# Performance work log

Hardware: AMD Instinct MI355X
Metric: run time of the kernel (lower is better)

## Reference

```python
import jax, jax.numpy as jnp
import numpy as np

B, N, C_IN, C_OUT = 32, 4096, 16, 64
EMB, LINK, WIN = 16, 3, 12


def setup_inputs() -> dict:
    key = jax.random.key(0)
    ks = jax.random.split(key, 7)
    s = lambda k, shape, sc=1.0: jax.random.normal(k, shape, dtype=jnp.float32) * sc
    return {
        "x": s(ks[0], (B, N, C_IN)),
        "x_window": s(ks[1], (B, WIN, N, C_IN)),
        "node_embeddings": s(ks[2], (N, EMB)),
        "weights_pool": s(ks[3], (EMB, LINK, C_IN, C_OUT), 0.1),
        "weights_window": s(ks[4], (EMB, C_IN, C_OUT), 0.1),
        "bias_pool": s(ks[5], (EMB, C_OUT), 0.1),
        "T": s(ks[6], (WIN,), 0.1),
    }


def reference(x, x_window, node_embeddings, weights_pool, weights_window, bias_pool, T):
    # Adaptive adjacency: softmax over rows of relu(E E^T)   [N, N]
    n = node_embeddings.shape[0]
    supports = jax.nn.softmax(
        jax.nn.relu(node_embeddings @ node_embeddings.T), axis=1)
    # Chebyshev polynomial hops: T0=I, T1=A, Tk = 2*A*T(k-1) - T(k-2)
    support_set = [jnp.eye(n, dtype=supports.dtype), supports]
    for _ in range(2, weights_pool.shape[1]):
        support_set.append(2.0 * (supports @ support_set[-1]) - support_set[-2])
    supports_k = jnp.stack(support_set, axis=0)  # [K, N, N]

    # Per-node weight generation from node embeddings
    weights = jnp.einsum('nd,dkio->nkio', node_embeddings, weights_pool)  # [N,K,Cin,Cout]
    bias = node_embeddings @ bias_pool  # [N, Cout]

    # Multi-hop spatial graph convolution
    x_g = jnp.einsum('knm,bmc->bnkc', supports_k, x)  # [B, N, K, Cin]
    x_gconv = jnp.einsum('bnki,nkio->bno', x_g, weights) + bias  # [B, N, Cout]

    # Temporal window transformation: time-mix with T, per-node weights
    x_w = jnp.einsum('btni,t->bni', x_window, T)  # [B, N, Cin]
    w_win = jnp.einsum('nd,dio->nio', node_embeddings, weights_window)  # [N,Cin,Cout]
    x_wconv = jnp.einsum('bni,nio->bno', x_w, w_win)  # [B, N, Cout]

    return x_gconv + x_wconv
```

## Files before the change

### kernel.cpp

```cpp
#include <hip/hip_runtime.h>
#include <hip/hip_bf16.h>

#define NN 4096
#define BB 32
#define CIN 16
#define COUT 64
#define EMB 16
#define KLINK 3
#define WWIN 12
#define BCIN (BB * CIN)
#define KSPLIT 4
#define KCHUNK (NN / KSPLIT)
#define NT (KCHUNK / 32)

typedef unsigned short ushort_t;
typedef __attribute__((ext_vector_type(8))) short bf16x8;
typedef __attribute__((ext_vector_type(4))) float f32x4;
typedef __attribute__((ext_vector_type(4))) unsigned short us4;
typedef __attribute__((ext_vector_type(8))) unsigned short us8;

static __device__ __forceinline__ ushort_t f2bf(float f) {
  union { float f; unsigned u; } v; v.f = f;
  const unsigned r = v.u + 0x7fffu + ((v.u >> 16) & 1u);
  return (ushort_t)(r >> 16);
}

__device__ __forceinline__ void gload16(const void* g, void* l) {
  __builtin_amdgcn_global_load_lds(
      (const __attribute__((address_space(1))) void*)g,
      (__attribute__((address_space(3))) void*)l, 16, 0, 0);
}

__global__ __launch_bounds__(256) void prep_kernel(
    const float* __restrict__ E, const float* __restrict__ Wp,
    const float* __restrict__ Wwp, const float* __restrict__ biasp,
    ushort_t* __restrict__ Ebf, ushort_t* __restrict__ Wpct,
    float* __restrict__ biasn, float* __restrict__ r) {
  const int gid = blockIdx.x * 256 + threadIdx.x;
  if (gid < NN) {
    r[gid] = 0.0f;
    const float* e = E + (size_t)gid * EMB;
    ushort_t* o = Ebf + (size_t)gid * 32;
    #pragma unroll
    for (int d = 0; d < 16; ++d) o[d] = f2bf(e[d]);
    #pragma unroll
    for (int d = 16; d < 32; ++d) o[d] = 0;
  } else if (gid < 2 * NN) {
    const int j = gid - NN;
    const int oo = j >> 6;
    const int i = j & 63;
    const int q = i >> 4;
    const int ii = i & 15;
    ushort_t* w = Wpct + (size_t)j * 32;
    #pragma unroll
    for (int d = 0; d < 16; ++d) {
      float v;
      if (q == 0)
        v = Wp[((size_t)(d * 3 + 0) * 16 + ii) * 64 + oo] -
            Wp[((size_t)(d * 3 + 2) * 16 + ii) * 64 + oo];
      else if (q == 1)
        v = Wp[((size_t)(d * 3 + 1) * 16 + ii) * 64 + oo];
      else if (q == 2)
        v = 2.0f * Wp[((size_t)(d * 3 + 2) * 16 + ii) * 64 + oo];
      else
        v = Wwp[((size_t)d * 16 + ii) * 64 + oo];
      w[d] = f2bf(v);
    }
    #pragma unroll
    for (int d = 16; d < 32; ++d) w[d] = 0;
  } else {
    const int t = gid - 2 * NN;
    if (t < NN * 16) {
      const int n = t >> 4;
      const int o4 = t & 15;
      const float4* bp4 = reinterpret_cast<const float4*>(biasp);
      float4 acc = make_float4(0.f, 0.f, 0.f, 0.f);
      #pragma unroll
      for (int d = 0; d < 16; ++d) {
        const float e = E[(size_t)n * EMB + d];
        const float4 b = bp4[d * 16 + o4];
        acc.x += e * b.x; acc.y += e * b.y; acc.z += e * b.z; acc.w += e * b.w;
      }
      *reinterpret_cast<float4*>(biasn + (size_t)n * 64 + o4 * 4) = acc;
    }
  }
}

__global__ __launch_bounds__(256) void uber_kernel(
    const ushort_t* __restrict__ Ebf, const ushort_t* __restrict__ Wpct,
    ushort_t* __restrict__ Wall, ushort_t* __restrict__ Pb,
    float* __restrict__ r,
    const float* __restrict__ x, const float* __restrict__ xw,
    const float* __restrict__ Tv,
    ushort_t* __restrict__ XtT, float* __restrict__ XW) {
  __shared__ ushort_t smem[6144];
  const int bid = blockIdx.x;
  const int tid = threadIdx.x;
  const int g = bid / 14;
  const int rm = bid - g * 14;

  if (rm < 4) {
    const int pidx = g * 4 + rm;
    const int row0 = (pidx >> 6) * 128;
    const int col0 = (pidx & 63) * 64;
    ushort_t* As = smem;
    ushort_t* Bs = smem + 4096;
    const int lane = tid & 63;
    const int wid = tid >> 6;
    const int wr = wid >> 1;
    const int wc = wid & 1;
    const int sr = tid >> 2;
    const int scs = (((tid & 3) ^ (sr & 3)) * 8);
    gload16(Ebf + (size_t)(row0 + sr) * 32 + scs, &As[tid * 8]);
    gload16(Ebf + (size_t)(row0 + 64 + sr) * 32 + scs, &As[2048 + tid * 8]);
    gload16(Ebf + (size_t)(col0 + sr) * 32 + scs, &Bs[tid * 8]);
    __syncthreads();

    const int kq = (lane >> 4) * 8;
    const int fr = lane & 15;
    bf16x8 af[4], bfr[2];
    #pragma unroll
    for (int i = 0; i < 4; ++i) {
      const int rr = wr * 64 + i * 16 + fr;
      af[i] = *reinterpret_cast<const bf16x8*>(&As[rr * 32 + (kq ^ ((rr & 3) * 8))]);
    }
    #pragma unroll
    for (int j = 0; j < 2; ++j) {
      const int rr = wc * 32 + j * 16 + fr;
      bfr[j] = *reinterpret_cast<const bf16x8*>(&Bs[rr * 32 + (kq ^ ((rr & 3) * 8))]);
    }
    f32x4 acc[4][2];
    #pragma unroll
    for (int i = 0; i < 4; ++i)
      #pragma unroll
      for (int j = 0; j < 2; ++j) acc[i][j] = (f32x4){0.f, 0.f, 0.f, 0.f};
    #pragma unroll
    for (int i = 0; i < 4; ++i)
      #pragma unroll
      for (int j = 0; j < 2; ++j)
        acc[i][j] = __builtin_amdgcn_mfma_f32_16x16x32_bf16(af[i], bfr[j],
                                                            acc[i][j], 0, 0, 0);
    float pv[4][2][4];
    #pragma unroll
    for (int i = 0; i < 4; ++i) {
      const int rg = row0 + wr * 64 + i * 16 + ((lane >> 4) << 2);
      #pragma unroll
      for (int j = 0; j < 2; ++j) {
        const int cg = col0 + wc * 32 + j * 16 + (lane & 15);
        us4 o;
        #pragma unroll
        for (int q = 0; q < 4; ++q) {
          const float p = __expf(fmaxf(acc[i][j][q], 0.0f) - 16.0f);
          pv[i][j][q] = p;
          o[q] = f2bf(p);
        }
        *reinterpret_cast<us4*>(&Pb[(size_t)cg * NN + rg]) = o;
      }
    }
    #pragma unroll
    for (int i = 0; i < 4; ++i) {
      const int rg = row0 + wr * 64 + i * 16 + ((lane >> 4) << 2);
      #pragma unroll
      for (int q = 0; q < 4; ++q) {
        float s = pv[i][0][q] + pv[i][1][q];
        s += __shfl_xor(s, 1, 64);
        s += __shfl_xor(s, 2, 64);
        s += __shfl_xor(s, 4, 64);
        s += __shfl_xor(s, 8, 64);
        if ((lane & 15) == 0) atomicAdd(&r[rg + q], s);
      }
    }
  } else if (rm < 8) {
    const int widx = g * 4 + (rm - 4);
    const int row0 = (widx >> 6) * 128;
    const int col0 = (widx & 63) * 64;
    ushort_t* As = smem;
    ushort_t* Bs = smem + 4096;
    const int lane = tid & 63;
    const int wid = tid >> 6;
    const int wr = wid >> 1;
    const int wc = wid & 1;
    const int sr = tid >> 2;
    const int scs = (((tid & 3) ^ (sr & 3)) * 8);
    gload16(Wpct + (size_t)(row0 + sr) * 32 + scs, &As[tid * 8]);
    gload16(Wpct + (size_t)(row0 + 64 + sr) * 32 + scs, &As[2048 + tid * 8]);
    gload16(Ebf + (size_t)(col0 + sr) * 32 + scs, &Bs[tid * 8]);
    __syncthreads();

    const int kq = (lane >> 4) * 8;
    const int fr = lane & 15;
    bf16x8 af[4], bfr[2];
    #pragma unroll
    for (int i = 0; i < 4; ++i) {
      const int rr = wr * 64 + i * 16 + fr;
      af[i] = *reinterpret_cast<const bf16x8*>(&As[rr * 32 + (kq ^ ((rr & 3) * 8))]);
    }
    #pragma unroll
    for (int j = 0; j < 2; ++j) {
      const int rr = wc * 32 + j * 16 + fr;
      bfr[j] = *reinterpret_cast<const bf16x8*>(&Bs[rr * 32 + (kq ^ ((rr & 3) * 8))]);
    }
    f32x4 acc[4][2];
    #pragma unroll
    for (int i = 0; i < 4; ++i)
      #pragma unroll
      for (int j = 0; j < 2; ++j) acc[i][j] = (f32x4){0.f, 0.f, 0.f, 0.f};
    #pragma unroll
    for (int i = 0; i < 4; ++i)
      #pragma unroll
      for (int j = 0; j < 2; ++j)
        acc[i][j] = __builtin_amdgcn_mfma_f32_16x16x32_bf16(af[i], bfr[j],
                                                            acc[i][j], 0, 0, 0);
    #pragma unroll
    for (int i = 0; i < 4; ++i) {
      const int rg = row0 + wr * 64 + i * 16 + ((lane >> 4) << 2);
      #pragma unroll
      for (int j = 0; j < 2; ++j) {
        const int cg = col0 + wc * 32 + j * 16 + (lane & 15);
        us4 o;
        o.x = f2bf(acc[i][j][0]);
        o.y = f2bf(acc[i][j][1]);
        o.z = f2bf(acc[i][j][2]);
        o.w = f2bf(acc[i][j][3]);
        *reinterpret_cast<us4*>(&Wall[(size_t)cg * NN + rg]) = o;
      }
    }
  } else if (rm < 10) {
    const int tidx = g * 2 + (rm - 8);
    const int lin = tidx * 256 + tid;
    const int c4 = (lin & 3) << 2;
    const int nn0 = ((lin >> 6) & 127) * 32 + ((lin >> 2) & 15);
    const int b = lin >> 13;
    float tv[WWIN];
    #pragma unroll
    for (int t = 0; t < WWIN; ++t) tv[t] = Tv[t];
    float4 a0 = make_float4(0.f, 0.f, 0.f, 0.f);
    float4 a1 = make_float4(0.f, 0.f, 0.f, 0.f);
    #pragma unroll 3
    for (int t = 0; t < WWIN; ++t) {
      const float4 v0 = *reinterpret_cast<const float4*>(
          xw + (((size_t)b * WWIN + t) * NN + nn0) * CIN + c4);
      const float4 v1 = *reinterpret_cast<const float4*>(
          xw + (((size_t)b * WWIN + t) * NN + nn0 + 16) * CIN + c4);
      a0.x += v0.x * tv[t]; a0.y += v0.y * tv[t];
      a0.z += v0.z * tv[t]; a0.w += v0.w * tv[t];
      a1.x += v1.x * tv[t]; a1.y += v1.y * tv[t];
      a1.z += v1.z * tv[t]; a1.w += v1.w * tv[t];
    }
    *reinterpret_cast<float4*>(XW + ((size_t)b * NN + nn0) * CIN + c4) = a0;
    *reinterpret_cast<float4*>(XW + ((size_t)b * NN + nn0 + 16) * CIN + c4) = a1;
  } else {
    const int txidx = g * 4 + (rm - 10);
    const int b = txidx >> 6;
    const int m0 = (txidx & 63) * 64;
    ushort_t (*T)[72] = reinterpret_cast<ushort_t(*)[72]>(smem);
    const int i = tid & 15;
    const int ml = tid >> 4;
    #pragma unroll
    for (int it = 0; it < 4; ++it) {
      const int m = m0 + ml + it * 16;
      T[i][ml + it * 16] = f2bf(x[((size_t)b * NN + m) * CIN + i]);
    }
    __syncthreads();
    if (tid < 128) {
      const int rr = tid >> 3;
      const int c8 = (tid & 7) * 8;
      const us8 v = *reinterpret_cast<const us8*>(&T[rr][c8]);
      *reinterpret_cast<us8*>(&XtT[(size_t)(b * CIN + rr) * NN + m0 + c8]) = v;
    }
  }
}

template <int CUR>
__device__ __forceinline__ void compute_tile(
    const ushort_t (&As)[3][128 * 32], const ushort_t (&Bs)[3][64 * 32],
    f32x4 (&acc)[4][2], int wr, int wc, int kq, int fr) {
  bf16x8 af[4], bfr[2];
  #pragma unroll
  for (int i = 0; i < 4; ++i) {
    const int rr = wr * 64 + i * 16 + fr;
    af[i] = *reinterpret_cast<const bf16x8*>(
        &As[CUR][rr * 32 + (kq ^ ((rr & 3) * 8))]);
  }
  #pragma unroll
  for (int j = 0; j < 2; ++j) {
    const int rr = wc * 32 + j * 16 + fr;
    bfr[j] = *reinterpret_cast<const bf16x8*>(
        &Bs[CUR][rr * 32 + (kq ^ ((rr & 3) * 8))]);
  }
  #pragma unroll
  for (int i = 0; i < 4; ++i)
    #pragma unroll
    for (int j = 0; j < 2; ++j)
      acc[i][j] = __builtin_amdgcn_mfma_f32_16x16x32_bf16(af[i], bfr[j],
                                                          acc[i][j], 0, 0, 0);
}

__global__ __launch_bounds__(256) void gemm_splitk_kernel(
    const ushort_t* __restrict__ Ag, const ushort_t* __restrict__ Bt,
    float* __restrict__ Cp, int lda, int ldb, int ldc) {
  __shared__ ushort_t As[3][128 * 32];
  __shared__ ushort_t Bs[3][64 * 32];
  const int tid = threadIdx.x;
  const int lane = tid & 63;
  const int wid = tid >> 6;
  const int wr = wid >> 1;
  const int wc = wid & 1;

  const int gx = gridDim.x, gy = gridDim.y;
  const int nwg = gx * gy * gridDim.z;
  int L = blockIdx.x + gx * (blockIdx.y + gy * blockIdx.z);
  L = (L & 7) * (nwg >> 3) + (L >> 3);
  const int bx = L % gx;
  const int by = (L / gx) % gy;
  const int bz = L / (gx * gy);

  const int row0 = by * 128;
  const int col0 = bx * 64;
  const int kbase = bz * KCHUNK;

  f32x4 acc[4][2];
  #pragma unroll
  for (int i = 0; i < 4; ++i)
    #pragma unroll
    for (int j = 0; j < 2; ++j) acc[i][j] = (f32x4){0.f, 0.f, 0.f, 0.f};

  const int sr = tid >> 2;
  const int scs = (((tid & 3) ^ (sr & 3)) * 8);
  const ushort_t* agp0 = Ag + (size_t)(row0 + sr) * lda + scs;
  const ushort_t* agp1 = Ag + (size_t)(row0 + 64 + sr) * lda + scs;
  const ushort_t* bgp  = Bt + (size_t)(col0 + sr) * ldb + scs;

  const int kq = (lane >> 4) * 8;
  const int fr = lane & 15;

#define STAGE(BUF, KB)                              \
  gload16(agp0 + (KB), &As[BUF][tid * 8]);          \
  gload16(agp1 + (KB), &As[BUF][2048 + tid * 8]);   \
  gload16(bgp + (KB), &Bs[BUF][tid * 8]);

#define PIPE_STEP(CUR, NB, TT)                                  \
  STAGE(NB, kbase + ((TT) + 2) * 32);                           \
  asm volatile("s_waitcnt vmcnt(6)" ::: "memory");              \
  __builtin_amdgcn_s_barrier();                                 \
  __builtin_amdgcn_sched_barrier(0);                            \
  compute_tile<CUR>(As, Bs, acc, wr, wc, kq, fr);               \
  __builtin_amdgcn_sched_barrier(0);                            \
  __builtin_amdgcn_s_barrier();

  STAGE(0, kbase);
  STAGE(1, kbase + 32);

  for (int tt = 0; tt < (NT - 2) / 3; ++tt) {
    const int t3 = tt * 3;
    PIPE_STEP(0, 2, t3 + 0);
    PIPE_STEP(1, 0, t3 + 1);
    PIPE_STEP(2, 1, t3 + 2);
  }
  asm volatile("s_waitcnt vmcnt(3)" ::: "memory");
  __builtin_amdgcn_s_barrier();
  __builtin_amdgcn_sched_barrier(0);
  compute_tile<0>(As, Bs, acc, wr, wc, kq, fr);
  __builtin_amdgcn_sched_barrier(0);
  __builtin_amdgcn_s_barrier();
  asm volatile("s_waitcnt vmcnt(0)" ::: "memory");
  __builtin_amdgcn_s_barrier();
  __builtin_amdgcn_sched_barrier(0);
  compute_tile<1>(As, Bs, acc, wr, wc, kq, fr);

#undef PIPE_STEP
#undef STAGE

  float* cpz = Cp + (size_t)bz * ((size_t)BCIN * NN);
  #pragma unroll
  for (int i = 0; i < 4; ++i) {
    const int rg = row0 + wr * 64 + i * 16 + ((lane >> 4) << 2);
    #pragma unroll
    for (int j = 0; j < 2; ++j) {
      const int cg = col0 + wc * 32 + j * 16 + (lane & 15);
      *reinterpret_cast<f32x4*>(&cpz[(size_t)cg * ldc + rg]) = acc[i][j];
    }
  }
}

__global__ __launch_bounds__(256) void reduce_y1_kernel(
    const float* __restrict__ Cp, const float* __restrict__ R,
    ushort_t* __restrict__ Y1T, ushort_t* __restrict__ Y1n) {
  __shared__ ushort_t T[64][72];
  const int n0 = blockIdx.x * 64;
  const int bc0 = blockIdx.y * 64;
  const int tid = threadIdx.x;
  const size_t SS = (size_t)BCIN * NN;
  #pragma unroll
  for (int q = 0; q < 4; ++q) {
    const int lin = tid + q * 256;
    const int bc = lin >> 4;
    const int nc = (lin & 15) * 4;
    const size_t base = (size_t)(bc0 + bc) * NN + n0 + nc;
    float4 s = *reinterpret_cast<const float4*>(Cp + base);
    #pragma unroll
    for (int z = 1; z < KSPLIT; ++z) {
      const float4 v = *reinterpret_cast<const float4*>(Cp + (size_t)z * SS + base);
      s.x += v.x; s.y += v.y; s.z += v.z; s.w += v.w;
    }
    const float4 rv = *reinterpret_cast<const float4*>(R + n0 + nc);
    us4 o;
    o.x = f2bf(s.x / rv.x); o.y = f2bf(s.y / rv.y);
    o.z = f2bf(s.z / rv.z); o.w = f2bf(s.w / rv.w);
    *reinterpret_cast<us4*>(&Y1T[base]) = o;
    *reinterpret_cast<us4*>(&T[bc][nc]) = o;
  }
  __syncthreads();
  #pragma unroll
  for (int t = 0; t < 2; ++t) {
    const int lin = tid + t * 256;
    const int nr = lin >> 3;
    const int ch = lin & 7;
    us8 v;
    #pragma unroll
    for (int e = 0; e < 8; ++e) v[e] = T[ch * 8 + e][nr];
    *reinterpret_cast<us8*>(&Y1n[(size_t)(n0 + nr) * BCIN + bc0 + ch * 8]) = v;
  }
}

__global__ __launch_bounds__(256) void reduce_y2_kernel(
    const float* __restrict__ Cp, ushort_t* __restrict__ Ct,
    const float* __restrict__ R) {
  const size_t e = ((size_t)blockIdx.x * 256 + threadIdx.x) << 2;
  const size_t SS = (size_t)BCIN * NN;
  float4 s = *reinterpret_cast<const float4*>(Cp + e);
  #pragma unroll
  for (int z = 1; z < KSPLIT; ++z) {
    const float4 v = *reinterpret_cast<const float4*>(Cp + (size_t)z * SS + e);
    s.x += v.x; s.y += v.y; s.z += v.z; s.w += v.w;
  }
  const float ri = 1.0f / R[e >> 9];
  s.x *= ri; s.y *= ri; s.z *= ri; s.w *= ri;
  us4 o;
  o.x = f2bf(s.x); o.y = f2bf(s.y); o.z = f2bf(s.z); o.w = f2bf(s.w);
  *reinterpret_cast<us4*>(Ct + e) = o;
}

__global__ __launch_bounds__(256) void combine_kernel(
    const float* __restrict__ x, const ushort_t* __restrict__ Y1n,
    const ushort_t* __restrict__ Y2n, const float* __restrict__ XW,
    const ushort_t* __restrict__ Wall, const float* __restrict__ biasn,
    float* __restrict__ out) {
  __shared__ ushort_t lds[4 * 6144];
  const int tid = threadIdx.x;
  const int lane = tid & 63;
  const int w = tid >> 6;
  ushort_t* Wl = lds + w * 6144;
  ushort_t* Vl = Wl + 4096;

  const int perm = ((lane >> 3) << 3) | ((lane & 7) ^ (lane >> 3));
  const int vb = lane >> 1;
  const int i0 = (lane & 1) * 8;

  for (int it = 0; it < 2; ++it) {
    const int n = blockIdx.x * 8 + w * 2 + it;
    asm volatile("s_waitcnt lgkmcnt(0)" ::: "memory");

    const ushort_t* wrow = Wall + (size_t)n * 4096;
    #pragma unroll
    for (int q = 0; q < 8; ++q)
      gload16(wrow + q * 512 + perm * 8, Wl + q * 512);

    const float4* xp = reinterpret_cast<const float4*>(
        x + ((size_t)vb * NN + n) * CIN + i0);
    const float4 xa = xp[0], xb = xp[1];
    const us8 y1 = *reinterpret_cast<const us8*>(Y1n + (size_t)n * BCIN + lane * 8);
    const us8 y2 = *reinterpret_cast<const us8*>(Y2n + (size_t)n * BCIN + lane * 8);
    const float4* xwp = reinterpret_cast<const float4*>(
        XW + ((size_t)vb * NN + n) * CIN + i0);
    const float4 wa = xwp[0], wb = xwp[1];
    us8 xv, wv;
    xv[0] = f2bf(xa.x); xv[1] = f2bf(xa.y); xv[2] = f2bf(xa.z); xv[3] = f2bf(xa.w);
    xv[4] = f2bf(xb.x); xv[5] = f2bf(xb.y); xv[6] = f2bf(xb.z); xv[7] = f2bf(xb.w);
    wv[0] = f2bf(wa.x); wv[1] = f2bf(wa.y); wv[2] = f2bf(wa.z); wv[3] = f2bf(wa.w);
    wv[4] = f2bf(wb.x); wv[5] = f2bf(wb.y); wv[6] = f2bf(wb.z); wv[7] = f2bf(wb.w);
    const int c0 = (lane & 1);
    const int vswz = vb & 7;
    *reinterpret_cast<us8*>(Vl + vb * 64 + (((c0 + 0) ^ vswz) << 3)) = xv;
    *reinterpret_cast<us8*>(Vl + vb * 64 + (((c0 + 2) ^ vswz) << 3)) = y1;
    *reinterpret_cast<us8*>(Vl + vb * 64 + (((c0 + 4) ^ vswz) << 3)) = y2;
    *reinterpret_cast<us8*>(Vl + vb * 64 + (((c0 + 6) ^ vswz) << 3)) = wv;

    f32x4 acc[2][4];
    #pragma unroll
    for (int nt = 0; nt < 4; ++nt) {
      const float bv = biasn[(size_t)n * 64 + nt * 16 + (lane & 15)];
      acc[0][nt] = (f32x4){bv, bv, bv, bv};
      acc[1][nt] = (f32x4){bv, bv, bv, bv};
    }

    asm volatile("s_waitcnt vmcnt(0)" ::: "memory");

    bf16x8 af[2][2], bfr[4][2];
    #pragma unroll
    for (int mt = 0; mt < 2; ++mt)
      #pragma unroll
      for (int kt = 0; kt < 2; ++kt) {
        const int rr = mt * 16 + (lane & 15);
        const int c = kt * 4 + (lane >> 4);
        af[mt][kt] = *reinterpret_cast<const bf16x8*>(
            Vl + rr * 64 + ((c ^ (lane & 7)) << 3));
      }
    #pragma unroll
    for (int nt = 0; nt < 4; ++nt)
      #pragma unroll
      for (int kt = 0; kt < 2; ++kt) {
        const int o = nt * 16 + (lane & 15);
        const int c = kt * 4 + (lane >> 4);
        bfr[nt][kt] = *reinterpret_cast<const bf16x8*>(
            Wl + o * 64 + ((c ^ (lane & 7)) << 3));
      }
    #pragma unroll
    for (int mt = 0; mt < 2; ++mt)
      #pragma unroll
      for (int nt = 0; nt < 4; ++nt)
        #pragma unroll
        for (int kt = 0; kt < 2; ++kt)
          acc[mt][nt] = __builtin_amdgcn_mfma_f32_16x16x32_bf16(
              af[mt][kt], bfr[nt][kt], acc[mt][nt], 0, 0, 0);

    #pragma unroll
    for (int mt = 0; mt < 2; ++mt)
      #pragma unroll
      for (int nt = 0; nt < 4; ++nt) {
        const int o = nt * 16 + (lane & 15);
        #pragma unroll
        for (int rr = 0; rr < 4; ++rr) {
          const int b = mt * 16 + ((lane >> 4) << 2) + rr;
          out[((size_t)b * NN + n) * COUT + o] = acc[mt][nt][rr];
        }
      }
  }
}

extern "C" void kernel_launch(void* const* d_in, const int* in_sizes, int n_in,
                              void* d_out, int out_size, void* d_ws,
                              size_t ws_size, hipStream_t stream) {
  const float* x = (const float*)d_in[0];
  const float* x_window = (const float*)d_in[1];
  const float* E = (const float*)d_in[2];
  const float* Wp = (const float*)d_in[3];
  const float* Wwp = (const float*)d_in[4];
  const float* biasp = (const float*)d_in[5];
  const float* Tv = (const float*)d_in[6];
  float* out = (float*)d_out;

  char* p = (char*)d_ws;
  float* XW = (float*)p;                 p += (size_t)BB * NN * CIN * 4;
  ushort_t* Pb = (ushort_t*)p;           p += (size_t)NN * NN * 2;
  ushort_t* XtT = (ushort_t*)p;          p += (size_t)BCIN * NN * 2;
  ushort_t* Y1T = (ushort_t*)p;          p += (size_t)BCIN * NN * 2;
  ushort_t* Y2n = (ushort_t*)p;          p += (size_t)NN * BCIN * 2;
  ushort_t* Y1n = (ushort_t*)p;          p += (size_t)NN * BCIN * 2;
  ushort_t* Wall = (ushort_t*)p;         p += (size_t)NN * 4096 * 2;
  ushort_t* Ebf = (ushort_t*)p;          p += (size_t)NN * 32 * 2;
  ushort_t* Wpct = (ushort_t*)p;         p += (size_t)NN * 32 * 2;
  float* biasn = (float*)p;              p += (size_t)NN * 64 * 4;
  float* r = (float*)p;                  p += (size_t)NN * 4;
  float* Cpart = (float*)p;              p += (size_t)KSPLIT * BCIN * NN * 4;

  prep_kernel<<<288, 256, 0, stream>>>(E, Wp, Wwp, biasp, Ebf, Wpct, biasn, r);
  uber_kernel<<<7168, 256, 0, stream>>>(Ebf, Wpct, Wall, Pb, r,
                                        x, x_window, Tv, XtT, XW);
  gemm_splitk_kernel<<<dim3(BCIN / 64, NN / 128, KSPLIT), 256, 0, stream>>>(
      Pb, XtT, Cpart, NN, NN, NN);
  reduce_y1_kernel<<<dim3(NN / 64, BCIN / 64), 256, 0, stream>>>(
      Cpart, r, Y1T, Y1n);
  gemm_splitk_kernel<<<dim3(NN / 64, BCIN / 128, KSPLIT), 256, 0, stream>>>(
      Y1T, Pb, Cpart, NN, NN, BCIN);
  reduce_y2_kernel<<<(BCIN * NN / 4) / 256, 256, 0, stream>>>(Cpart, Y2n, r);
  combine_kernel<<<NN / 8, 256, 0, stream>>>(x, Y1n, Y2n, XW, Wall, biasn, out);
}
```

Before: 180.4 us.

## Move temporal window mixing from uber kernel into the two split-K GEMM launches

The x_window time-mix, which is memory-bound and reads the largest input, leaves the uber kernel and is interleaved into both split-K GEMM kernels. In each, every third block does a slice of it instead of a GEMM tile. The aim is to overlap that bandwidth-heavy streaming with the compute-heavy MFMA GEMM tiles and to shorten the uber kernel. The GEMM grid becomes 1D with a hardcoded block remap (`*128`) that assumes 1024 GEMM tiles. Mixing blocks with different resource profiles may hurt GEMM scheduling or cache behaviour.

```diff
diff --git a/kernel.cpp b/kernel.cpp
--- a/kernel.cpp
+++ b/kernel.cpp
@@ -90,14 +90,12 @@
     const ushort_t* __restrict__ Ebf, const ushort_t* __restrict__ Wpct,
     ushort_t* __restrict__ Wall, ushort_t* __restrict__ Pb,
     float* __restrict__ r,
-    const float* __restrict__ x, const float* __restrict__ xw,
-    const float* __restrict__ Tv,
-    ushort_t* __restrict__ XtT, float* __restrict__ XW) {
+    const float* __restrict__ x, ushort_t* __restrict__ XtT) {
   __shared__ ushort_t smem[6144];
   const int bid = blockIdx.x;
   const int tid = threadIdx.x;
-  const int g = bid / 14;
-  const int rm = bid - g * 14;
+  const int g = bid / 12;
+  const int rm = bid - g * 12;
 
   if (rm < 4) {
     const int pidx = g * 4 + rm;
@@ -225,9 +223,66 @@
         *reinterpret_cast<us4*>(&Wall[(size_t)cg * NN + rg]) = o;
       }
     }
-  } else if (rm < 10) {
-    const int tidx = g * 2 + (rm - 8);
-    const int lin = tidx * 256 + tid;
+  } else {
+    const int txidx = g * 4 + (rm - 8);
+    const int b = txidx >> 6;
+    const int m0 = (txidx & 63) * 64;
+    ushort_t (*T)[72] = reinterpret_cast<ushort_t(*)[72]>(smem);
+    const int i = tid & 15;
+    const int ml = tid >> 4;
+    #pragma unroll
+    for (int it = 0; it < 4; ++it) {
+      const int m = m0 + ml + it * 16;
+      T[i][ml + it * 16] = f2bf(x[((size_t)b * NN + m) * CIN + i]);
+    }
+    __syncthreads();
+    if (tid < 128) {
+      const int rr = tid >> 3;
+      const int c8 = (tid & 7) * 8;
+      const us8 v = *reinterpret_cast<const us8*>(&T[rr][c8]);
+      *reinterpret_cast<us8*>(&XtT[(size_t)(b * CIN + rr) * NN + m0 + c8]) = v;
+    }
+  }
+}
+
+template <int CUR>
+__device__ __forceinline__ void compute_tile(
+    const ushort_t (&As)[3][128 * 32], const ushort_t (&Bs)[3][64 * 32],
+    f32x4 (&acc)[4][2], int wr, int wc, int kq, int fr) {
+  bf16x8 af[4], bfr[2];
+  #pragma unroll
+  for (int i = 0; i < 4; ++i) {
+    const int rr = wr * 64 + i * 16 + fr;
+    af[i] = *reinterpret_cast<const bf16x8*>(
+        &As[CUR][rr * 32 + (kq ^ ((rr & 3) * 8))]);
+  }
+  #pragma unroll
+  for (int j = 0; j < 2; ++j) {
+    const int rr = wc * 32 + j * 16 + fr;
+    bfr[j] = *reinterpret_cast<const bf16x8*>(
+        &Bs[CUR][rr * 32 + (kq ^ ((rr & 3) * 8))]);
+  }
+  #pragma unroll
+  for (int i = 0; i < 4; ++i)
+    #pragma unroll
+    for (int j = 0; j < 2; ++j)
+      acc[i][j] = __builtin_amdgcn_mfma_f32_16x16x32_bf16(af[i], bfr[j],
+                                                          acc[i][j], 0, 0, 0);
+}
+
+__global__ __launch_bounds__(256) void gemm_splitk_tm_kernel(
+    const ushort_t* __restrict__ Ag, const ushort_t* __restrict__ Bt,
+    float* __restrict__ Cp, int lda, int ldb, int ldc, int gx, int gy,
+    const float* __restrict__ xw, const float* __restrict__ Tv,
+    float* __restrict__ XW, int tmBase) {
+  __shared__ ushort_t As[3][128 * 32];
+  __shared__ ushort_t Bs[3][64 * 32];
+  const int tid = threadIdx.x;
+  const int g = blockIdx.x / 3;
+  const int rm = blockIdx.x - g * 3;
+
+  if (rm == 2) {
+    const int lin = (tmBase + g) * 256 + tid;
     const int c4 = (lin & 3) << 2;
     const int nn0 = ((lin >> 6) & 127) * 32 + ((lin >> 2) & 15);
     const int b = lin >> 13;
@@ -249,68 +304,16 @@
     }
     *reinterpret_cast<float4*>(XW + ((size_t)b * NN + nn0) * CIN + c4) = a0;
     *reinterpret_cast<float4*>(XW + ((size_t)b * NN + nn0 + 16) * CIN + c4) = a1;
-  } else {
-    const int txidx = g * 4 + (rm - 10);
-    const int b = txidx >> 6;
-    const int m0 = (txidx & 63) * 64;
-    ushort_t (*T)[72] = reinterpret_cast<ushort_t(*)[72]>(smem);
-    const int i = tid & 15;
-    const int ml = tid >> 4;
-    #pragma unroll
-    for (int it = 0; it < 4; ++it) {
-      const int m = m0 + ml + it * 16;
-      T[i][ml + it * 16] = f2bf(x[((size_t)b * NN + m) * CIN + i]);
-    }
-    __syncthreads();
-    if (tid < 128) {
-      const int rr = tid >> 3;
-      const int c8 = (tid & 7) * 8;
-      const us8 v = *reinterpret_cast<const us8*>(&T[rr][c8]);
-      *reinterpret_cast<us8*>(&XtT[(size_t)(b * CIN + rr) * NN + m0 + c8]) = v;
-    }
-  }
-}
-
-template <int CUR>
-__device__ __forceinline__ void compute_tile(
-    const ushort_t (&As)[3][128 * 32], const ushort_t (&Bs)[3][64 * 32],
-    f32x4 (&acc)[4][2], int wr, int wc, int kq, int fr) {
-  bf16x8 af[4], bfr[2];
-  #pragma unroll
-  for (int i = 0; i < 4; ++i) {
-    const int rr = wr * 64 + i * 16 + fr;
-    af[i] = *reinterpret_cast<const bf16x8*>(
-        &As[CUR][rr * 32 + (kq ^ ((rr & 3) * 8))]);
-  }
-  #pragma unroll
-  for (int j = 0; j < 2; ++j) {
-    const int rr = wc * 32 + j * 16 + fr;
-    bfr[j] = *reinterpret_cast<const bf16x8*>(
-        &Bs[CUR][rr * 32 + (kq ^ ((rr & 3) * 8))]);
-  }
-  #pragma unroll
-  for (int i = 0; i < 4; ++i)
-    #pragma unroll
-    for (int j = 0; j < 2; ++j)
-      acc[i][j] = __builtin_amdgcn_mfma_f32_16x16x32_bf16(af[i], bfr[j],
-                                                          acc[i][j], 0, 0, 0);
-}
-
-__global__ __launch_bounds__(256) void gemm_splitk_kernel(
-    const ushort_t* __restrict__ Ag, const ushort_t* __restrict__ Bt,
-    float* __restrict__ Cp, int lda, int ldb, int ldc) {
-  __shared__ ushort_t As[3][128 * 32];
-  __shared__ ushort_t Bs[3][64 * 32];
-  const int tid = threadIdx.x;
+    return;
+  }
+
   const int lane = tid & 63;
   const int wid = tid >> 6;
   const int wr = wid >> 1;
   const int wc = wid & 1;
 
-  const int gx = gridDim.x, gy = gridDim.y;
-  const int nwg = gx * gy * gridDim.z;
-  int L = blockIdx.x + gx * (blockIdx.y + gy * blockIdx.z);
-  L = (L & 7) * (nwg >> 3) + (L >> 3);
+  const int sid = g * 2 + rm;
+  const int L = (sid & 7) * 128 + (sid >> 3);
   const int bx = L % gx;
   const int by = (L / gx) % gy;
   const int bz = L / (gx * gy);
@@ -565,14 +568,15 @@
   float* Cpart = (float*)p;              p += (size_t)KSPLIT * BCIN * NN * 4;
 
   prep_kernel<<<288, 256, 0, stream>>>(E, Wp, Wwp, biasp, Ebf, Wpct, biasn, r);
-  uber_kernel<<<7168, 256, 0, stream>>>(Ebf, Wpct, Wall, Pb, r,
-                                        x, x_window, Tv, XtT, XW);
-  gemm_splitk_kernel<<<dim3(BCIN / 64, NN / 128, KSPLIT), 256, 0, stream>>>(
-      Pb, XtT, Cpart, NN, NN, NN);
+  uber_kernel<<<6144, 256, 0, stream>>>(Ebf, Wpct, Wall, Pb, r, x, XtT);
+  gemm_splitk_tm_kernel<<<1536, 256, 0, stream>>>(
+      Pb, XtT, Cpart, NN, NN, NN, BCIN / 64, NN / 128,
+      x_window, Tv, XW, 0);
   reduce_y1_kernel<<<dim3(NN / 64, BCIN / 64), 256, 0, stream>>>(
       Cpart, r, Y1T, Y1n);
-  gemm_splitk_kernel<<<dim3(NN / 64, BCIN / 128, KSPLIT), 256, 0, stream>>>(
-      Y1T, Pb, Cpart, NN, NN, BCIN);
+  gemm_splitk_tm_kernel<<<1536, 256, 0, stream>>>(
+      Y1T, Pb, Cpart, NN, NN, BCIN, NN / 64, BCIN / 128,
+      x_window, Tv, XW, 512);
   reduce_y2_kernel<<<(BCIN * NN / 4) / 256, 256, 0, stream>>>(Cpart, Y2n, r);
   combine_kernel<<<NN / 8, 256, 0, stream>>>(x, Y1n, Y2n, XW, Wall, biasn, out);
 }
```

After: 201.5 us. +11.7%, slower.

## Fuse split-K Y2 reduction into combine kernel, nontemporal x_window loads

Applied to the files above, without the earlier changes.

Removes the separate reduce_y2 kernel and performs the split-K partial sum, normalization by R, and bf16 conversion directly inside combine_kernel when it loads Y2 per node. This eliminates one launch plus the write and re-read of the bf16 Y2n buffer. Combine now reads the fp32 partials (4x larger than bf16) directly, which adds latency to that kernel. Separately, the streaming x_window loads in the temporal-mix path now use nontemporal loads to avoid polluting cache.

```diff
diff --git a/kernel.cpp b/kernel.cpp
--- a/kernel.cpp
+++ b/kernel.cpp
@@ -29,6 +29,11 @@
   __builtin_amdgcn_global_load_lds(
       (const __attribute__((address_space(1))) void*)g,
       (__attribute__((address_space(3))) void*)l, 16, 0, 0);
+}
+
+__device__ __forceinline__ float4 nt_load4(const float* p) {
+  const f32x4 v = __builtin_nontemporal_load(reinterpret_cast<const f32x4*>(p));
+  return make_float4(v[0], v[1], v[2], v[3]);
 }
 
 __global__ __launch_bounds__(256) void prep_kernel(
@@ -238,9 +243,9 @@
     float4 a1 = make_float4(0.f, 0.f, 0.f, 0.f);
     #pragma unroll 3
     for (int t = 0; t < WWIN; ++t) {
-      const float4 v0 = *reinterpret_cast<const float4*>(
+      const float4 v0 = nt_load4(
           xw + (((size_t)b * WWIN + t) * NN + nn0) * CIN + c4);
-      const float4 v1 = *reinterpret_cast<const float4*>(
+      const float4 v1 = nt_load4(
           xw + (((size_t)b * WWIN + t) * NN + nn0 + 16) * CIN + c4);
       a0.x += v0.x * tv[t]; a0.y += v0.y * tv[t];
       a0.z += v0.z * tv[t]; a0.w += v0.w * tv[t];
@@ -423,27 +428,10 @@
   }
 }
 
-__global__ __launch_bounds__(256) void reduce_y2_kernel(
-    const float* __restrict__ Cp, ushort_t* __restrict__ Ct,
-    const float* __restrict__ R) {
-  const size_t e = ((size_t)blockIdx.x * 256 + threadIdx.x) << 2;
-  const size_t SS = (size_t)BCIN * NN;
-  float4 s = *reinterpret_cast<const float4*>(Cp + e);
-  #pragma unroll
-  for (int z = 1; z < KSPLIT; ++z) {
-    const float4 v = *reinterpret_cast<const float4*>(Cp + (size_t)z * SS + e);
-    s.x += v.x; s.y += v.y; s.z += v.z; s.w += v.w;
-  }
-  const float ri = 1.0f / R[e >> 9];
-  s.x *= ri; s.y *= ri; s.z *= ri; s.w *= ri;
-  us4 o;
-  o.x = f2bf(s.x); o.y = f2bf(s.y); o.z = f2bf(s.z); o.w = f2bf(s.w);
-  *reinterpret_cast<us4*>(Ct + e) = o;
-}
-
 __global__ __launch_bounds__(256) void combine_kernel(
     const float* __restrict__ x, const ushort_t* __restrict__ Y1n,
-    const ushort_t* __restrict__ Y2n, const float* __restrict__ XW,
+    const float* __restrict__ Cp2, const float* __restrict__ R,
+    const float* __restrict__ XW,
     const ushort_t* __restrict__ Wall, const float* __restrict__ biasn,
     float* __restrict__ out) {
   __shared__ ushort_t lds[4 * 6144];
@@ -452,6 +440,7 @@
   const int w = tid >> 6;
   ushort_t* Wl = lds + w * 6144;
   ushort_t* Vl = Wl + 4096;
+  const size_t SS = (size_t)BCIN * NN;
 
   const int perm = ((lane >> 3) << 3) | ((lane & 7) ^ (lane >> 3));
   const int vb = lane >> 1;
@@ -470,7 +459,24 @@
         x + ((size_t)vb * NN + n) * CIN + i0);
     const float4 xa = xp[0], xb = xp[1];
     const us8 y1 = *reinterpret_cast<const us8*>(Y1n + (size_t)n * BCIN + lane * 8);
-    const us8 y2 = *reinterpret_cast<const us8*>(Y2n + (size_t)n * BCIN + lane * 8);
+
+    const float* cp2 = Cp2 + (size_t)n * BCIN + lane * 8;
+    float4 s0 = *reinterpret_cast<const float4*>(cp2);
+    float4 s1 = *reinterpret_cast<const float4*>(cp2 + 4);
+    #pragma unroll
+    for (int z = 1; z < KSPLIT; ++z) {
+      const float4 v0 = *reinterpret_cast<const float4*>(cp2 + (size_t)z * SS);
+      const float4 v1 = *reinterpret_cast<const float4*>(cp2 + (size_t)z * SS + 4);
+      s0.x += v0.x; s0.y += v0.y; s0.z += v0.z; s0.w += v0.w;
+      s1.x += v1.x; s1.y += v1.y; s1.z += v1.z; s1.w += v1.w;
+    }
+    const float ri = 1.0f / R[n];
+    us8 y2;
+    y2[0] = f2bf(s0.x * ri); y2[1] = f2bf(s0.y * ri);
+    y2[2] = f2bf(s0.z * ri); y2[3] = f2bf(s0.w * ri);
+    y2[4] = f2bf(s1.x * ri); y2[5] = f2bf(s1.y * ri);
+    y2[6] = f2bf(s1.z * ri); y2[7] = f2bf(s1.w * ri);
+
     const float4* xwp = reinterpret_cast<const float4*>(
         XW + ((size_t)vb * NN + n) * CIN + i0);
     const float4 wa = xwp[0], wb = xwp[1];
@@ -555,7 +561,6 @@
   ushort_t* Pb = (ushort_t*)p;           p += (size_t)NN * NN * 2;
   ushort_t* XtT = (ushort_t*)p;          p += (size_t)BCIN * NN * 2;
   ushort_t* Y1T = (ushort_t*)p;          p += (size_t)BCIN * NN * 2;
-  ushort_t* Y2n = (ushort_t*)p;          p += (size_t)NN * BCIN * 2;
   ushort_t* Y1n = (ushort_t*)p;          p += (size_t)NN * BCIN * 2;
   ushort_t* Wall = (ushort_t*)p;         p += (size_t)NN * 4096 * 2;
   ushort_t* Ebf = (ushort_t*)p;          p += (size_t)NN * 32 * 2;
@@ -573,6 +578,6 @@
       Cpart, r, Y1T, Y1n);
   gemm_splitk_kernel<<<dim3(NN / 64, BCIN / 128, KSPLIT), 256, 0, stream>>>(
       Y1T, Pb, Cpart, NN, NN, BCIN);
-  reduce_y2_kernel<<<(BCIN * NN / 4) / 256, 256, 0, stream>>>(Cpart, Y2n, r);
-  combine_kernel<<<NN / 8, 256, 0, stream>>>(x, Y1n, Y2n, XW, Wall, biasn, out);
-}
+  combine_kernel<<<NN / 8, 256, 0, stream>>>(x, Y1n, Cpart, r, XW,
+                                             Wall, biasn, out);
+}
```

New measurement: 174.9 us (median of 2 runs). 3.1% less time.
